# Kernel tuning notes

Hardware: AMD Instinct MI355X
Metric: run time of the kernel (lower is better)

Reference implementation:

```python
import jax, jax.numpy as jnp
import numpy as np

HH = 38  # sqrt(amd0=1444)
KD = 3   # 3x3 neighborhood


def setup_inputs() -> dict:
    key = jax.random.key(0)
    fm = jax.random.normal(key, (16, 512, HH, HH), dtype=jnp.float32)
    return {"fm": fm}


def reference(fm):
    # fm: [B, C, H, W] -> replication pad 1 -> NHWC -> gather 3x3 neighbors,
    # concatenated along the channel axis in row-major neighbor order
    # (matching counts[:, 0..8] = (h-1,w-1),(h-1,w),(h-1,w+1),(h,w-1),...).
    B, C, H, W = fm.shape
    x = jnp.pad(fm, ((0, 0), (0, 0), (1, 1), (1, 1)), mode="edge")  # [B,C,H+2,W+2]
    x = jnp.transpose(x, (0, 2, 3, 1))  # [B, H+2, W+2, C]
    patches = [x[:, di:di + H, dj:dj + W, :] for di in range(KD) for dj in range(KD)]
    pfm = jnp.concatenate(patches, axis=-1)  # [B, H, W, 9*C]
    return pfm.reshape(B, H * W, KD * KD * C)  # [B, 1444, 9*C]
```

## Files before the change

### kernel.cpp

```cpp
#include <hip/hip_runtime.h>


#define BB 16
#define CC 512
#define HH 38
#define WW 38
#define HW (HH * WW)
#define KK 9
#define CCH 128
#define NCH (CC / CCH)
#define LC (CCH + 4)
#define NTHREADS 512

__global__ __launch_bounds__(NTHREADS) void spatial_pool_kernel(
    const float* __restrict__ fm, float* __restrict__ out)
{
    __shared__ float lds[3][WW][LC];

    const int blk   = blockIdx.x;
    const int chunk = blk & (NCH - 1);
    const int bh    = blk >> 2;
    const int h     = bh % HH;
    const int b     = bh / HH;
    const int c0    = chunk * CCH;

    const int r0 = (h - 1 < 0) ? 0 : h - 1;
    const int r1 = h;
    const int r2 = (h + 1 > HH - 1) ? HH - 1 : h + 1;

    const float* base = fm + ((size_t)b * CC + c0) * HW;
    const int NL2 = 3 * CCH * (WW / 2);
    for (int idx = threadIdx.x; idx < NL2; idx += NTHREADS) {
        int w2 = idx % (WW / 2);
        int rc = idx / (WW / 2);
        int c  = rc & (CCH - 1);
        int r  = rc >> 7;
        int hr = (r == 0) ? r0 : ((r == 1) ? r1 : r2);
        const float2 v = *(const float2*)(base + c * HW + hr * WW + 2 * w2);
        lds[r][2 * w2 + 0][c] = v.x;
        lds[r][2 * w2 + 1][c] = v.y;
    }
    __syncthreads();

    float4* outb4 = (float4*)(out + (((size_t)b * HW + (size_t)h * WW) * KK) * CC + c0);
    const int NST4 = WW * KK * (CCH / 4);
    for (int i = threadIdx.x; i < NST4; i += NTHREADS) {
        int c4 = i & 31;
        int wk = i >> 5;
        int w  = wk / KK;
        int k  = wk - w * KK;
        int di = k / 3;
        int dj = k - di * 3;
        int wp = w + dj - 1;
        wp = (wp < 0) ? 0 : ((wp > WW - 1) ? WW - 1 : wp);
        const float4 v = *(const float4*)&lds[di][wp][c4 * 4];
        outb4[(size_t)wk * (CC / 4) + c4] = v;
    }
}

extern "C" void kernel_launch(void* const* d_in, const int* in_sizes, int n_in,
                              void* d_out, int out_size, void* d_ws, size_t ws_size,
                              hipStream_t stream) {
    const float* fm = (const float*)d_in[0];
    float* out = (float*)d_out;
    dim3 grid(BB * HH * NCH);
    dim3 block(NTHREADS);
    spatial_pool_kernel<<<grid, block, 0, stream>>>(fm, out);
}
```

Before: 460.3 us.

## Split into NCHW-to-NHWC transpose pass plus flat 9-neighbor gather kernel

Replaces the single fused kernel with two passes: the first transposes the input once into NHWC in the workspace, and the second is a grid-stride gather that copies float4 rows from that buffer into the 9x-expanded output. The goal is to stop re-reading each input row three times through LDS with strided NCHW loads. Each output element now comes from a contiguous NHWC read that should mostly hit cache. The cost is an extra write and read of a full NHWC intermediate, a second launch, and per-element integer divisions in the gather. The old fused kernel is kept as a fallback for when the workspace is too small.

```diff
diff --git a/kernel.cpp b/kernel.cpp
--- a/kernel.cpp
+++ b/kernel.cpp
@@ -10,13 +10,12 @@
 #define CCH 128
 #define NCH (CC / CCH)
 #define LC (CCH + 4)
-#define NTHREADS 512
+#define NT 512
 
-__global__ __launch_bounds__(NTHREADS) void spatial_pool_kernel(
-    const float* __restrict__ fm, float* __restrict__ out)
+__global__ __launch_bounds__(NT) void nchw_to_nhwc(const float* __restrict__ fm,
+                                                   float* __restrict__ nhwc)
 {
-    __shared__ float lds[3][WW][LC];
-
+    __shared__ float lds[WW][LC];
     const int blk   = blockIdx.x;
     const int chunk = blk & (NCH - 1);
     const int bh    = blk >> 2;
@@ -24,13 +23,67 @@
     const int b     = bh / HH;
     const int c0    = chunk * CCH;
 
+    const float* base = fm + ((size_t)b * CC + c0) * HW + h * WW;
+    const int NL2 = CCH * (WW / 2);
+    for (int idx = threadIdx.x; idx < NL2; idx += NT) {
+        int w2 = idx % (WW / 2);
+        int c  = idx / (WW / 2);
+        const float2 v = *(const float2*)(base + c * HW + 2 * w2);
+        lds[2 * w2 + 0][c] = v.x;
+        lds[2 * w2 + 1][c] = v.y;
+    }
+    __syncthreads();
+    float4* dst = (float4*)(nhwc + ((size_t)b * HW + (size_t)h * WW) * CC + c0);
+    const int NS = WW * (CCH / 4);
+    for (int i = threadIdx.x; i < NS; i += NT) {
+        int c4 = i & 31;
+        int w  = i >> 5;
+        dst[(size_t)w * (CC / 4) + c4] = *(const float4*)&lds[w][c4 * 4];
+    }
+}
+
+__global__ __launch_bounds__(NT) void gather9(const float* __restrict__ nhwc,
+                                              float4* __restrict__ out4)
+{
+    const int NF4 = BB * HW * KK * (CC / 4);
+    const float4* src = (const float4*)nhwc;
+    int f = blockIdx.x * NT + threadIdx.x;
+    const int c4 = f & 127;
+    int r = f >> 7;
+    const int stride_f = gridDim.x * NT;
+    const int stride_r = stride_f >> 7;
+    for (; f < NF4; f += stride_f, r += stride_r) {
+        unsigned ur = (unsigned)r;
+        unsigned q  = ur / 9u;
+        unsigned k  = ur - q * 9u;
+        unsigned b  = q / (unsigned)HW;
+        unsigned hw = q - b * (unsigned)HW;
+        unsigned h  = hw / (unsigned)WW;
+        unsigned w  = hw - h * (unsigned)WW;
+        unsigned di = k / 3u;
+        unsigned dj = k - 3u * di;
+        int hp = (int)h + (int)di - 1; hp = hp < 0 ? 0 : (hp > HH - 1 ? HH - 1 : hp);
+        int wp = (int)w + (int)dj - 1; wp = wp < 0 ? 0 : (wp > WW - 1 ? WW - 1 : wp);
+        out4[f] = src[((size_t)b * HW + (size_t)hp * WW + wp) * (CC / 4) + c4];
+    }
+}
+
+__global__ __launch_bounds__(NT) void spatial_pool_fallback(
+    const float* __restrict__ fm, float* __restrict__ out)
+{
+    __shared__ float lds[3][WW][LC];
+    const int blk   = blockIdx.x;
+    const int chunk = blk & (NCH - 1);
+    const int bh    = blk >> 2;
+    const int h     = bh % HH;
+    const int b     = bh / HH;
+    const int c0    = chunk * CCH;
     const int r0 = (h - 1 < 0) ? 0 : h - 1;
     const int r1 = h;
     const int r2 = (h + 1 > HH - 1) ? HH - 1 : h + 1;
-
     const float* base = fm + ((size_t)b * CC + c0) * HW;
     const int NL2 = 3 * CCH * (WW / 2);
-    for (int idx = threadIdx.x; idx < NL2; idx += NTHREADS) {
+    for (int idx = threadIdx.x; idx < NL2; idx += NT) {
         int w2 = idx % (WW / 2);
         int rc = idx / (WW / 2);
         int c  = rc & (CCH - 1);
@@ -41,10 +94,9 @@
         lds[r][2 * w2 + 1][c] = v.y;
     }
     __syncthreads();
-
     float4* outb4 = (float4*)(out + (((size_t)b * HW + (size_t)h * WW) * KK) * CC + c0);
     const int NST4 = WW * KK * (CCH / 4);
-    for (int i = threadIdx.x; i < NST4; i += NTHREADS) {
+    for (int i = threadIdx.x; i < NST4; i += NT) {
         int c4 = i & 31;
         int wk = i >> 5;
         int w  = wk / KK;
@@ -53,8 +105,7 @@
         int dj = k - di * 3;
         int wp = w + dj - 1;
         wp = (wp < 0) ? 0 : ((wp > WW - 1) ? WW - 1 : wp);
-        const float4 v = *(const float4*)&lds[di][wp][c4 * 4];
-        outb4[(size_t)wk * (CC / 4) + c4] = v;
+        outb4[(size_t)wk * (CC / 4) + c4] = *(const float4*)&lds[di][wp][c4 * 4];
     }
 }
 
@@ -63,7 +114,12 @@
                               hipStream_t stream) {
     const float* fm = (const float*)d_in[0];
     float* out = (float*)d_out;
-    dim3 grid(BB * HH * NCH);
-    dim3 block(NTHREADS);
-    spatial_pool_kernel<<<grid, block, 0, stream>>>(fm, out);
+    const size_t NHWC_BYTES = (size_t)BB * HW * CC * sizeof(float);
+    if (ws_size >= NHWC_BYTES) {
+        float* nhwc = (float*)d_ws;
+        nchw_to_nhwc<<<BB * HH * NCH, NT, 0, stream>>>(fm, nhwc);
+        gather9<<<2432, NT, 0, stream>>>(nhwc, (float4*)out);
+    } else {
+        spatial_pool_fallback<<<BB * HH * NCH, NT, 0, stream>>>(fm, out);
+    }
 }
```

Result: slower. 497.1 us (+8.0%).
